# Kernel tuning notes

Hardware: AMD Instinct MI355X
Metric: run time of the kernel (lower is better)

## Reference

```python
import jax, jax.numpy as jnp
import numpy as np

MARGIN = 0.3
BIG = 10000.0  # sentinel used by the original when a gt/lt negative set is empty


def setup_inputs() -> dict:
    key = jax.random.key(0)
    k1, k2 = jax.random.split(key)
    inputs = jax.random.normal(k1, (4096, 256), dtype=jnp.float32)
    targets = jax.random.randint(k2, (4096,), 0, 4, dtype=jnp.int32)
    return {"inputs": inputs, "targets": targets}


def reference(inputs, targets):
    # Pairwise Euclidean distance matrix (n, n).
    sq = jnp.sum(inputs * inputs, axis=1)
    d2 = sq[:, None] + sq[None, :] - 2.0 * (inputs @ inputs.T)
    dist = jnp.sqrt(jnp.maximum(d2, 0.0))

    # mask[i, j] semantics from the torch code (rows of expand are `targets`):
    #   eq: targets[j] == targets[i]; gt: targets[j] > targets[i]; lt: targets[j] < targets[i]
    eq = targets[None, :] == targets[:, None]
    gt = targets[None, :] > targets[:, None]
    lt = targets[None, :] < targets[:, None]

    # Hardest positive: max distance over same-label columns (diag always eq -> non-empty).
    hard_ap = jnp.max(jnp.where(eq, dist, -jnp.inf), axis=1)
    # Hardest greater / less negatives: min distance, sentinel BIG when set empty.
    an_g = jnp.min(jnp.where(gt, dist, jnp.inf), axis=1)
    an_g = jnp.where(jnp.isinf(an_g), BIG, an_g)
    an_l = jnp.min(jnp.where(lt, dist, jnp.inf), axis=1)
    an_l = jnp.where(jnp.isinf(an_l), BIG, an_l)

    loss = jnp.mean(jax.nn.relu(hard_ap - jnp.abs(an_g - an_l) + MARGIN))
    # cnt: rows whose positive set is just the anchor itself
    cnt = jnp.sum(jnp.sum(eq, axis=1) == 1)
    return loss, dist, cnt
```

## Files before the change

### kernel.cpp

```cpp
#include <hip/hip_runtime.h>

#define N 4096
#define D 256
#define MARGIN 0.3f
#define BIG 10000.0f

typedef _Float16 f16x8 __attribute__((ext_vector_type(8)));
typedef _Float16 f16x4 __attribute__((ext_vector_type(4)));
typedef float floatx16 __attribute__((ext_vector_type(16)));

__device__ inline void atomicMaxFloatPos(float* a, float v) {
    atomicMax((int*)a, __float_as_int(v));
}
__device__ inline void atomicMinFloatPos(float* a, float v) {
    atomicMin((int*)a, __float_as_int(v));
}

__device__ inline void gl_lds16(const void* g, void* l) {
    __builtin_amdgcn_global_load_lds(
        (const __attribute__((address_space(1))) unsigned int*)g,
        (__attribute__((address_space(3))) unsigned int*)l, 16, 0, 0);
}

__global__ __launch_bounds__(256) void prep_kernel(const float* __restrict__ x,
                                                   float* __restrict__ sq,
                                                   _Float16* __restrict__ Xf,
                                                   float* ap, float* ang, float* anl) {
    const int wave = threadIdx.x >> 6, lane = threadIdx.x & 63;
    const int row = blockIdx.x * 4 + wave;
    const float4 v = *(const float4*)(x + (size_t)row * D + lane * 4);
    f16x4 h;
    h[0] = (_Float16)v.x; h[1] = (_Float16)v.y;
    h[2] = (_Float16)v.z; h[3] = (_Float16)v.w;
    *(f16x4*)(Xf + (size_t)row * D + lane * 4) = h;
    const float c0 = (float)h[0], c1 = (float)h[1], c2 = (float)h[2], c3 = (float)h[3];
    float s = c0 * c0 + c1 * c1 + c2 * c2 + c3 * c3;
    #pragma unroll
    for (int off = 32; off; off >>= 1) s += __shfl_down(s, off);
    if (lane == 0) sq[row] = s;
    if (threadIdx.x < 4) {
        const int i = blockIdx.x * 4 + threadIdx.x;
        ap[i] = 0.0f; ang[i] = BIG; anl[i] = BIG;
    }
}

__global__ __launch_bounds__(512, 2) void dist_kernel(const _Float16* __restrict__ Xf,
                                                      const int* __restrict__ tgt,
                                                      const float* __restrict__ sq,
                                                      float* __restrict__ dist,
                                                      float* ap, float* ang, float* anl) {
    __shared__ _Float16 lds[65536];

    const int tid  = threadIdx.x;
    const int wv   = tid >> 6;
    const int lane = tid & 63;
    const int row0 = blockIdx.y * 256;
    const int col0 = blockIdx.x * 256;
    const int wr = wv >> 2, wc = wv & 3;

    const int g = lane >> 3, p = lane & 7, lq = p ^ g;
    const int base_row = (wv < 4 ? row0 : col0) + (wv & 3) * 64 + g;
    const _Float16* src0 = Xf + (size_t)base_row * D + lq * 8;
    const int dstoff = ((wv & 4) ? 16384 : 0) + (wv & 3) * 4096;

    const int m0 = lane & 31;
    const int hi = lane >> 5;
    const int sw = m0 & 7;

    floatx16 acc[4][2];
    #pragma unroll
    for (int mt = 0; mt < 4; ++mt)
        #pragma unroll
        for (int nt = 0; nt < 2; ++nt)
            #pragma unroll
            for (int r = 0; r < 16; ++r) acc[mt][nt][r] = 0.0f;

    #define ISSUE_STAGE(s)                                                        \
    do {                                                                          \
        _Float16* buf_ = lds + ((s) & 1) * 32768;                                 \
        const int k0_ = (s) * 64;                                                 \
        _Pragma("unroll")                                                         \
        for (int d = 0; d < 8; ++d)                                               \
            gl_lds16(src0 + (size_t)d * 8 * D + k0_, buf_ + dstoff + d * 512);    \
    } while (0)

    ISSUE_STAGE(0);

    #pragma unroll
    for (int s = 0; s < 4; ++s) {
        if (s < 3) ISSUE_STAGE(s + 1);
        if (s < 3) { __asm__ volatile("s_waitcnt vmcnt(8)" ::: "memory"); }
        else       { __asm__ volatile("s_waitcnt vmcnt(0)" ::: "memory"); }
        __builtin_amdgcn_s_barrier();
        __asm__ volatile("" ::: "memory");

        const _Float16* buf   = lds + (s & 1) * 32768;
        const _Float16* Abase = buf + ((size_t)wr * 8192 + m0 * 64);
        const _Float16* Bbase = buf + 16384 + ((size_t)wc * 4096 + m0 * 64);

        __builtin_amdgcn_s_setprio(1);
        #pragma unroll
        for (int kb = 0; kb < 4; ++kb) {
            const int po = (((kb * 2 + hi) ^ sw) << 3);
            f16x8 b0 = *(const f16x8*)(Bbase + po);
            f16x8 b1 = *(const f16x8*)(Bbase + 2048 + po);
            #pragma unroll
            for (int mt = 0; mt < 4; ++mt) {
                f16x8 a = *(const f16x8*)(Abase + mt * 2048 + po);
                acc[mt][0] = __builtin_amdgcn_mfma_f32_32x32x16_f16(a, b0, acc[mt][0], 0, 0, 0);
                acc[mt][1] = __builtin_amdgcn_mfma_f32_32x32x16_f16(a, b1, acc[mt][1], 0, 0, 0);
            }
        }
        __builtin_amdgcn_s_setprio(0);

        if (s < 2) {
            __asm__ volatile("" ::: "memory");
            __builtin_amdgcn_s_barrier();
            __asm__ volatile("" ::: "memory");
        }
    }
    #undef ISSUE_STAGE

    const int rowA    = row0 + wr * 128;
    const int colbase = col0 + wc * 64;
    const int tl0 = tgt[rowA + lane];
    const int tl1 = tgt[rowA + 64 + lane];
    const float sqr0 = sq[rowA + lane];
    const float sqr1 = sq[rowA + 64 + lane];
    const unsigned long long pa0 = __ballot(tl0 & 1), pa1 = __ballot(tl0 & 2);
    const unsigned long long pb0 = __ballot(tl1 & 1), pb1 = __ballot(tl1 & 2);
    const int gc0 = colbase + m0, gc1 = colbase + 32 + m0;
    const int tc0 = tgt[gc0], tc1 = tgt[gc1];
    const float sqc0 = sq[gc0], sqc1 = sq[gc1];
    const int rl_base = 4 * hi;

    float mx0 = 0.0f, mg0 = BIG, ml0 = BIG;
    float mx1 = 0.0f, mg1 = BIG, ml1 = BIG;

    #pragma unroll
    for (int mt = 0; mt < 4; ++mt) {
        #pragma unroll
        for (int r = 0; r < 16; ++r) {
            const int row_l = mt * 32 + (r & 3) + 8 * (r >> 2) + rl_base;
            const int rl = row_l & 63;
            const int grow = rowA + row_l;
            const float sqi = __shfl(mt < 2 ? sqr0 : sqr1, rl);
            const float d0 = sqrtf(fmaxf(sqi + sqc0 - 2.0f * acc[mt][0][r], 0.0f));
            const float d1 = sqrtf(fmaxf(sqi + sqc1 - 2.0f * acc[mt][1][r], 0.0f));
            __builtin_nontemporal_store(d0, dist + (size_t)grow * N + gc0);
            __builtin_nontemporal_store(d1, dist + (size_t)grow * N + gc1);
            const unsigned long long q0 = (mt < 2 ? pa0 : pb0);
            const unsigned long long q1 = (mt < 2 ? pa1 : pb1);
            const int tr = (int)((q0 >> rl) & 1) | ((int)((q1 >> rl) & 1) << 1);
            mx0 = fmaxf(mx0, (tr == tc0) ? d0 : 0.0f);
            mg0 = fminf(mg0, (tr >  tc0) ? d0 : BIG);
            ml0 = fminf(ml0, (tr <  tc0) ? d0 : BIG);
            mx1 = fmaxf(mx1, (tr == tc1) ? d1 : 0.0f);
            mg1 = fminf(mg1, (tr >  tc1) ? d1 : BIG);
            ml1 = fminf(ml1, (tr <  tc1) ? d1 : BIG);
        }
    }
    mx0 = fmaxf(mx0, __shfl_xor(mx0, 32));
    mg0 = fminf(mg0, __shfl_xor(mg0, 32));
    ml0 = fminf(ml0, __shfl_xor(ml0, 32));
    mx1 = fmaxf(mx1, __shfl_xor(mx1, 32));
    mg1 = fminf(mg1, __shfl_xor(mg1, 32));
    ml1 = fminf(ml1, __shfl_xor(ml1, 32));

    if (hi == 0) {
        atomicMaxFloatPos(&ap[gc0],  mx0);
        atomicMinFloatPos(&ang[gc0], mg0);
        atomicMinFloatPos(&anl[gc0], ml0);
        atomicMaxFloatPos(&ap[gc1],  mx1);
        atomicMinFloatPos(&ang[gc1], mg1);
        atomicMinFloatPos(&anl[gc1], ml1);
    }
}

__global__ __launch_bounds__(1024) void finish_kernel(const float* __restrict__ ap,
                                                      const float* __restrict__ ang,
                                                      const float* __restrict__ anl,
                                                      const int* __restrict__ tgt,
                                                      float* __restrict__ out) {
    __shared__ int hist[4];
    __shared__ unsigned hsum[2][16];
    __shared__ float wsum[16];
    __shared__ int wcnt[16];
    const int tid = threadIdx.x, lane = tid & 63, wv = tid >> 6;

    const int4 t4 = *(const int4*)&tgt[tid * 4];
    int c[4] = {0, 0, 0, 0};
    c[t4.x & 3]++; c[t4.y & 3]++; c[t4.z & 3]++; c[t4.w & 3]++;
    unsigned p01 = (unsigned)c[0] | ((unsigned)c[1] << 16);
    unsigned p23 = (unsigned)c[2] | ((unsigned)c[3] << 16);
    #pragma unroll
    for (int off = 32; off; off >>= 1) {
        p01 += __shfl_down(p01, off);
        p23 += __shfl_down(p23, off);
    }
    if (lane == 0) { hsum[0][wv] = p01; hsum[1][wv] = p23; }
    __syncthreads();
    if (tid == 0) {
        unsigned a = 0, b = 0;
        for (int i = 0; i < 16; ++i) { a += hsum[0][i]; b += hsum[1][i]; }
        hist[0] = a & 0xFFFF; hist[1] = a >> 16;
        hist[2] = b & 0xFFFF; hist[3] = b >> 16;
    }
    __syncthreads();

    float term = 0.0f; int cc = 0;
    const int lab[4] = {t4.x & 3, t4.y & 3, t4.z & 3, t4.w & 3};
    #pragma unroll
    for (int j = 0; j < 4; ++j) {
        const int i = tid * 4 + j;
        term += fmaxf(ap[i] - fabsf(ang[i] - anl[i]) + MARGIN, 0.0f);
        cc += (hist[lab[j]] == 1) ? 1 : 0;
    }
    #pragma unroll
    for (int off = 32; off; off >>= 1) {
        term += __shfl_down(term, off);
        cc   += __shfl_down(cc, off);
    }
    if (lane == 0) { wsum[wv] = term; wcnt[wv] = cc; }
    __syncthreads();
    if (tid == 0) {
        float ls = 0.0f; int cs = 0;
        for (int i = 0; i < 16; ++i) { ls += wsum[i]; cs += wcnt[i]; }
        out[0] = ls * (1.0f / N);
        out[1 + (size_t)N * N] = (float)cs;
    }
}

extern "C" void kernel_launch(void* const* d_in, const int* in_sizes, int n_in,
                              void* d_out, int out_size, void* d_ws, size_t ws_size,
                              hipStream_t stream) {
    const float* x   = (const float*)d_in[0];
    const int*   tgt = (const int*)d_in[1];
    float* out = (float*)d_out;
    char*  ws  = (char*)d_ws;

    _Float16* Xf  = (_Float16*)ws;
    float*    sq  = (float*)(ws + 2097152);
    float*    ap  = sq + 4096;
    float*    ang = sq + 8192;
    float*    anl = sq + 12288;

    prep_kernel<<<N / 4, 256, 0, stream>>>(x, sq, Xf, ap, ang, anl);
    dim3 grid(N / 256, N / 256);
    dist_kernel<<<grid, 512, 0, stream>>>(Xf, tgt, sq, out + 1, ap, ang, anl);
    finish_kernel<<<1, 1024, 0, stream>>>(ap, ang, anl, tgt, out);
}
```

Baseline: 108.9 us.

## Deepen GEMM K-pipeline to four 32-wide stages and parallelize finish reduction

The distance GEMM now streams K in eight 32-wide stages through a four-buffer LDS ring with three stages in flight. Each stage is loaded cooperatively by all waves into an interleaved A/B layout, and the trailing barrier per stage is removed. Launch bounds drop to one block per SM. The finish kernel is split across 16 blocks that combine results with atomic adds into outputs zeroed by the prep kernel, which cuts the serial single-block tail. In exchange the GEMM has more barriers and waits per tile, and float atomics make the summation order nondeterministic.

```diff
diff --git a/kernel.cpp b/kernel.cpp
--- a/kernel.cpp
+++ b/kernel.cpp
@@ -25,7 +25,8 @@
 __global__ __launch_bounds__(256) void prep_kernel(const float* __restrict__ x,
                                                    float* __restrict__ sq,
                                                    _Float16* __restrict__ Xf,
-                                                   float* ap, float* ang, float* anl) {
+                                                   float* ap, float* ang, float* anl,
+                                                   float* __restrict__ out) {
     const int wave = threadIdx.x >> 6, lane = threadIdx.x & 63;
     const int row = blockIdx.x * 4 + wave;
     const float4 v = *(const float4*)(x + (size_t)row * D + lane * 4);
@@ -42,9 +43,13 @@
         const int i = blockIdx.x * 4 + threadIdx.x;
         ap[i] = 0.0f; ang[i] = BIG; anl[i] = BIG;
     }
-}
-
-__global__ __launch_bounds__(512, 2) void dist_kernel(const _Float16* __restrict__ Xf,
+    if (blockIdx.x == 0 && threadIdx.x == 0) {
+        out[0] = 0.0f;
+        out[1 + (size_t)N * N] = 0.0f;
+    }
+}
+
+__global__ __launch_bounds__(512, 1) void dist_kernel(const _Float16* __restrict__ Xf,
                                                       const int* __restrict__ tgt,
                                                       const float* __restrict__ sq,
                                                       float* __restrict__ dist,
@@ -59,9 +64,8 @@
     const int wr = wv >> 2, wc = wv & 3;
 
     const int g = lane >> 3, p = lane & 7, lq = p ^ g;
-    const int base_row = (wv < 4 ? row0 : col0) + (wv & 3) * 64 + g;
-    const _Float16* src0 = Xf + (size_t)base_row * D + lq * 8;
-    const int dstoff = ((wv & 4) ? 16384 : 0) + (wv & 3) * 4096;
+    const int sel  = (lq < 4 ? row0 : col0) + g;
+    const int koff = (lq & 3) * 8;
 
     const int m0 = lane & 31;
     const int hi = lane >> 5;
@@ -75,49 +79,51 @@
             #pragma unroll
             for (int r = 0; r < 16; ++r) acc[mt][nt][r] = 0.0f;
 
-    #define ISSUE_STAGE(s)                                                        \
+    #define ISSUE_STAGE(st)                                                       \
     do {                                                                          \
-        _Float16* buf_ = lds + ((s) & 1) * 32768;                                 \
-        const int k0_ = (s) * 64;                                                 \
+        _Float16* buf_ = lds + ((st) & 3) * 16384;                                \
+        const int k0_ = (st) * 32;                                                \
         _Pragma("unroll")                                                         \
-        for (int d = 0; d < 8; ++d)                                               \
-            gl_lds16(src0 + (size_t)d * 8 * D + k0_, buf_ + dstoff + d * 512);    \
+        for (int d = 0; d < 4; ++d) {                                             \
+            const int rg = wv * 4 + d;                                            \
+            gl_lds16(Xf + (size_t)(sel + rg * 8) * D + k0_ + koff,                \
+                     buf_ + rg * 512);                                            \
+        }                                                                         \
     } while (0)
 
     ISSUE_STAGE(0);
-
-    #pragma unroll
-    for (int s = 0; s < 4; ++s) {
-        if (s < 3) ISSUE_STAGE(s + 1);
-        if (s < 3) { __asm__ volatile("s_waitcnt vmcnt(8)" ::: "memory"); }
-        else       { __asm__ volatile("s_waitcnt vmcnt(0)" ::: "memory"); }
+    ISSUE_STAGE(1);
+    ISSUE_STAGE(2);
+
+    #pragma unroll
+    for (int s = 0; s < 8; ++s) {
+        if (s < 6)      { __asm__ volatile("s_waitcnt vmcnt(8)" ::: "memory"); }
+        else if (s == 6){ __asm__ volatile("s_waitcnt vmcnt(4)" ::: "memory"); }
+        else            { __asm__ volatile("s_waitcnt vmcnt(0)" ::: "memory"); }
         __builtin_amdgcn_s_barrier();
-        __asm__ volatile("" ::: "memory");
-
-        const _Float16* buf   = lds + (s & 1) * 32768;
-        const _Float16* Abase = buf + ((size_t)wr * 8192 + m0 * 64);
-        const _Float16* Bbase = buf + 16384 + ((size_t)wc * 4096 + m0 * 64);
+        if (s < 5) ISSUE_STAGE(s + 3);
+
+        const _Float16* buf = lds + (s & 3) * 16384;
+        const _Float16* Ab  = buf + ((size_t)wr * 128 + m0) * 64;
+        const _Float16* Bb  = buf + ((size_t)wc * 64  + m0) * 64;
 
         __builtin_amdgcn_s_setprio(1);
         #pragma unroll
-        for (int kb = 0; kb < 4; ++kb) {
-            const int po = (((kb * 2 + hi) ^ sw) << 3);
-            f16x8 b0 = *(const f16x8*)(Bbase + po);
-            f16x8 b1 = *(const f16x8*)(Bbase + 2048 + po);
+        for (int ks = 0; ks < 2; ++ks) {
+            const int la  = ks * 2 + hi;
+            const int poa = ((la       ^ sw) << 3);
+            const int pob = (((la + 4) ^ sw) << 3);
+            f16x8 b0 = *(const f16x8*)(Bb + pob);
+            f16x8 b1 = *(const f16x8*)(Bb + 2048 + pob);
             #pragma unroll
             for (int mt = 0; mt < 4; ++mt) {
-                f16x8 a = *(const f16x8*)(Abase + mt * 2048 + po);
+                f16x8 a = *(const f16x8*)(Ab + mt * 2048 + poa);
                 acc[mt][0] = __builtin_amdgcn_mfma_f32_32x32x16_f16(a, b0, acc[mt][0], 0, 0, 0);
                 acc[mt][1] = __builtin_amdgcn_mfma_f32_32x32x16_f16(a, b1, acc[mt][1], 0, 0, 0);
             }
         }
         __builtin_amdgcn_s_setprio(0);
-
-        if (s < 2) {
-            __asm__ volatile("" ::: "memory");
-            __builtin_amdgcn_s_barrier();
-            __asm__ volatile("" ::: "memory");
-        }
+        __asm__ volatile("" ::: "memory");
     }
     #undef ISSUE_STAGE
 
@@ -177,20 +183,22 @@
     }
 }
 
-__global__ __launch_bounds__(1024) void finish_kernel(const float* __restrict__ ap,
-                                                      const float* __restrict__ ang,
-                                                      const float* __restrict__ anl,
-                                                      const int* __restrict__ tgt,
-                                                      float* __restrict__ out) {
-    __shared__ int hist[4];
-    __shared__ unsigned hsum[2][16];
-    __shared__ float wsum[16];
-    __shared__ int wcnt[16];
+__global__ __launch_bounds__(256) void finish_kernel(const float* __restrict__ ap,
+                                                     const float* __restrict__ ang,
+                                                     const float* __restrict__ anl,
+                                                     const int* __restrict__ tgt,
+                                                     float* __restrict__ out) {
+    __shared__ unsigned hs01[4], hs23[4];
+    __shared__ float fs[4];
+    __shared__ int   cs[4];
     const int tid = threadIdx.x, lane = tid & 63, wv = tid >> 6;
 
-    const int4 t4 = *(const int4*)&tgt[tid * 4];
     int c[4] = {0, 0, 0, 0};
-    c[t4.x & 3]++; c[t4.y & 3]++; c[t4.z & 3]++; c[t4.w & 3]++;
+    #pragma unroll
+    for (int j = 0; j < 4; ++j) {
+        const int4 t4 = *(const int4*)&tgt[(j * 256 + tid) * 4];
+        c[t4.x & 3]++; c[t4.y & 3]++; c[t4.z & 3]++; c[t4.w & 3]++;
+    }
     unsigned p01 = (unsigned)c[0] | ((unsigned)c[1] << 16);
     unsigned p23 = (unsigned)c[2] | ((unsigned)c[3] << 16);
     #pragma unroll
@@ -198,36 +206,30 @@
         p01 += __shfl_down(p01, off);
         p23 += __shfl_down(p23, off);
     }
-    if (lane == 0) { hsum[0][wv] = p01; hsum[1][wv] = p23; }
+    if (lane == 0) { hs01[wv] = p01; hs23[wv] = p23; }
     __syncthreads();
-    if (tid == 0) {
-        unsigned a = 0, b = 0;
-        for (int i = 0; i < 16; ++i) { a += hsum[0][i]; b += hsum[1][i]; }
-        hist[0] = a & 0xFFFF; hist[1] = a >> 16;
-        hist[2] = b & 0xFFFF; hist[3] = b >> 16;
-    }
-    __syncthreads();
-
-    float term = 0.0f; int cc = 0;
-    const int lab[4] = {t4.x & 3, t4.y & 3, t4.z & 3, t4.w & 3};
-    #pragma unroll
-    for (int j = 0; j < 4; ++j) {
-        const int i = tid * 4 + j;
-        term += fmaxf(ap[i] - fabsf(ang[i] - anl[i]) + MARGIN, 0.0f);
-        cc += (hist[lab[j]] == 1) ? 1 : 0;
-    }
+    const unsigned a = hs01[0] + hs01[1] + hs01[2] + hs01[3];
+    const unsigned b = hs23[0] + hs23[1] + hs23[2] + hs23[3];
+    const int h0 = a & 0xFFFF, h1 = a >> 16, h2 = b & 0xFFFF, h3 = b >> 16;
+
+    const int row = blockIdx.x * 256 + tid;
+    const int t = tgt[row] & 3;
+    float term = fmaxf(ap[row] - fabsf(ang[row] - anl[row]) + MARGIN, 0.0f);
+    const int h = (t == 0) ? h0 : (t == 1) ? h1 : (t == 2) ? h2 : h3;
+    int cc = (h == 1) ? 1 : 0;
+
     #pragma unroll
     for (int off = 32; off; off >>= 1) {
         term += __shfl_down(term, off);
         cc   += __shfl_down(cc, off);
     }
-    if (lane == 0) { wsum[wv] = term; wcnt[wv] = cc; }
+    if (lane == 0) { fs[wv] = term; cs[wv] = cc; }
     __syncthreads();
     if (tid == 0) {
-        float ls = 0.0f; int cs = 0;
-        for (int i = 0; i < 16; ++i) { ls += wsum[i]; cs += wcnt[i]; }
-        out[0] = ls * (1.0f / N);
-        out[1 + (size_t)N * N] = (float)cs;
+        const float ls = fs[0] + fs[1] + fs[2] + fs[3];
+        const int   csum = cs[0] + cs[1] + cs[2] + cs[3];
+        atomicAdd(&out[0], ls * (1.0f / N));
+        atomicAdd(&out[1 + (size_t)N * N], (float)csum);
     }
 }
 
@@ -245,8 +247,8 @@
     float*    ang = sq + 8192;
     float*    anl = sq + 12288;
 
-    prep_kernel<<<N / 4, 256, 0, stream>>>(x, sq, Xf, ap, ang, anl);
+    prep_kernel<<<N / 4, 256, 0, stream>>>(x, sq, Xf, ap, ang, anl, out);
     dim3 grid(N / 256, N / 256);
     dist_kernel<<<grid, 512, 0, stream>>>(Xf, tgt, sq, out + 1, ap, ang, anl);
-    finish_kernel<<<1, 1024, 0, stream>>>(ap, ang, anl, tgt, out);
-}
+    finish_kernel<<<16, 256, 0, stream>>>(ap, ang, anl, tgt, out);
+}
```

Measured after the change: 107.6 us. Within noise of the previous version (-1.1%).
